# Performance work log

Hardware: AMD Instinct MI355X
Metric: run time of the kernel (lower is better)

The kernel has to match this reference:

```python
import jax, jax.numpy as jnp
import numpy as np

E = 384      # dim_embd
H = 6        # n_heads
D = E // H   # head dim = 64
T_MAX = 256  # block_size
EPS = 1e-5


def setup_inputs() -> dict:
    key = jax.random.key(0)
    ks = jax.random.split(key, 12)
    B, T = 128, 256
    s_in = (1.0 / E) ** 0.5
    s_ff = (1.0 / (4 * E)) ** 0.5
    return {
        "x": jax.random.normal(ks[0], (B, T, E), jnp.float32),
        # per-head projections stacked to match torch concat order: [E, H*D]
        "wq": jax.random.normal(ks[1], (E, E), jnp.float32) * s_in,
        "wk": jax.random.normal(ks[2], (E, E), jnp.float32) * s_in,
        "wv": jax.random.normal(ks[3], (E, E), jnp.float32) * s_in,
        "w_proj": jax.random.normal(ks[4], (E, E), jnp.float32) * s_in,
        "b_proj": jnp.zeros((E,), jnp.float32),
        "w1": jax.random.normal(ks[5], (E, 4 * E), jnp.float32) * s_in,
        "b1": jnp.zeros((4 * E,), jnp.float32),
        "w2": jax.random.normal(ks[6], (4 * E, E), jnp.float32) * s_ff,
        "b2": jnp.zeros((E,), jnp.float32),
        "g1": jnp.ones((E,), jnp.float32),
        "beta1": jnp.zeros((E,), jnp.float32),
        "g2": jnp.ones((E,), jnp.float32),
        "beta2": jnp.zeros((E,), jnp.float32),
    }


def _layernorm(x, g, b):
    mu = jnp.mean(x, axis=-1, keepdims=True)
    var = jnp.mean(jnp.square(x - mu), axis=-1, keepdims=True)
    return (x - mu) * jax.lax.rsqrt(var + EPS) * g + b


def _attention(x, wq, wk, wv, w_proj, b_proj):
    B, T, C = x.shape
    # batched per-head projections: [B,T,H,D]
    q = (x @ wq).reshape(B, T, H, D)
    k = (x @ wk).reshape(B, T, H, D)
    v = (x @ wv).reshape(B, T, H, D)
    # NOTE: original scales by C**-0.5 with C = full embed dim (384)
    scale = C ** (-0.5)
    scores = jnp.einsum("bthd,bshd->bhts", q, k) * scale
    mask = jnp.tril(jnp.ones((T, T), bool))
    scores = jnp.where(mask, scores, -jnp.inf)
    wei = jax.nn.softmax(scores, axis=-1)  # dropout = identity (eval)
    out = jnp.einsum("bhts,bshd->bthd", wei, v).reshape(B, T, C)
    return out @ w_proj + b_proj


def reference(x, wq, wk, wv, w_proj, b_proj, w1, b1, w2, b2, g1, beta1, g2, beta2):
    x = x + _attention(_layernorm(x, g1, beta1), wq, wk, wv, w_proj, b_proj)
    h = _layernorm(x, g2, beta2)
    h = jax.nn.relu(h @ w1 + b1) @ w2 + b2  # dropout = identity (eval)
    return x + h
```

## Files before the change

### kernel.cpp

```cpp
#include <hip/hip_runtime.h>
#include <hip/hip_bf16.h>

typedef __attribute__((ext_vector_type(8))) short bf16x8;
typedef __attribute__((ext_vector_type(4))) float f32x4;

#define MFMA_BF16(a, b, c) __builtin_amdgcn_mfma_f32_16x16x32_bf16((a), (b), (c), 0, 0, 0)

#define E_DIM 384
#define T_SEQ 256
#define B_BATCH 128
#define H_HEADS 6
#define D_HEAD 64
#define NROWS (B_BATCH * T_SEQ)
#define FF_DIM (4 * E_DIM)
#define QKV_LD 1152

__device__ __forceinline__ void load_lds16(const __hip_bfloat16* g, __hip_bfloat16* l) {
    __builtin_amdgcn_global_load_lds(
        (const __attribute__((address_space(1))) void*)g,
        (__attribute__((address_space(3))) void*)l, 16, 0, 0);
}

__device__ __forceinline__ float to_f(float x) { return x; }
__device__ __forceinline__ float to_f(__hip_bfloat16 x) { return __bfloat162float(x); }

__global__ void tcast_all_kernel(const float* __restrict__ wq, const float* __restrict__ wk,
                                 const float* __restrict__ wv, const float* __restrict__ wp,
                                 const float* __restrict__ w1, const float* __restrict__ w2,
                                 __hip_bfloat16* __restrict__ wqkvT, __hip_bfloat16* __restrict__ wpT,
                                 __hip_bfloat16* __restrict__ w1T, __hip_bfloat16* __restrict__ w2T) {
    const int WE = E_DIM * E_DIM;
    const int FE = E_DIM * FF_DIM;
    int idx = blockIdx.x * 256 + threadIdx.x;
    if (idx < 3 * WE) {
        int seg = idx / WE, j = idx - seg * WE;
        const float* W = seg == 0 ? wq : (seg == 1 ? wk : wv);
        int k = j / E_DIM, n = j - k * E_DIM;
        wqkvT[(size_t)seg * WE + (size_t)n * E_DIM + k] = __float2bfloat16(W[j]);
    } else if (idx < 4 * WE) {
        int j = idx - 3 * WE;
        int k = j / E_DIM, n = j - k * E_DIM;
        wpT[(size_t)n * E_DIM + k] = __float2bfloat16(wp[j]);
    } else if (idx < 4 * WE + FE) {
        int j = idx - 4 * WE;
        int k = j / FF_DIM, n = j - k * FF_DIM;
        w1T[(size_t)n * E_DIM + k] = __float2bfloat16(w1[j]);
    } else {
        int j = idx - 4 * WE - FE;
        int k = j / E_DIM, n = j - k * E_DIM;
        w2T[(size_t)n * FF_DIM + k] = __float2bfloat16(w2[j]);
    }
}

template <typename TI>
__global__ __launch_bounds__(256) void ln_kernel(const TI* __restrict__ x,
                                                 const float* __restrict__ g,
                                                 const float* __restrict__ bta,
                                                 __hip_bfloat16* __restrict__ out) {
    int row = blockIdx.x * 4 + (threadIdx.x >> 6);
    int lane = threadIdx.x & 63;
    const TI* xr = x + (size_t)row * E_DIM;
    float vals[6];
    float s = 0.f;
#pragma unroll
    for (int i = 0; i < 3; i++) {
        int c = i * 128 + 2 * lane;
        if constexpr (sizeof(TI) == 4) {
            float2 v = *reinterpret_cast<const float2*>(&xr[c]);
            vals[2 * i] = v.x;
            vals[2 * i + 1] = v.y;
        } else {
            ushort2 u = *reinterpret_cast<const ushort2*>(&xr[c]);
            union { unsigned short us; __hip_bfloat16 h; } a, b2;
            a.us = u.x; b2.us = u.y;
            vals[2 * i] = __bfloat162float(a.h);
            vals[2 * i + 1] = __bfloat162float(b2.h);
        }
        s += vals[2 * i] + vals[2 * i + 1];
    }
#pragma unroll
    for (int off = 1; off < 64; off <<= 1) s += __shfl_xor(s, off, 64);
    float mu = s * (1.f / E_DIM);
    float vv = 0.f;
#pragma unroll
    for (int i = 0; i < 6; i++) {
        float d = vals[i] - mu;
        vv += d * d;
    }
#pragma unroll
    for (int off = 1; off < 64; off <<= 1) vv += __shfl_xor(vv, off, 64);
    float rstd = rsqrtf(vv * (1.f / E_DIM) + 1e-5f);
#pragma unroll
    for (int i = 0; i < 3; i++) {
        int c = i * 128 + 2 * lane;
        float2 gv = *reinterpret_cast<const float2*>(&g[c]);
        float2 bv = *reinterpret_cast<const float2*>(&bta[c]);
        union { ushort2 u; struct { __hip_bfloat16 a, b; } h; } o2;
        o2.h.a = __float2bfloat16((vals[2 * i] - mu) * rstd * gv.x + bv.x);
        o2.h.b = __float2bfloat16((vals[2 * i + 1] - mu) * rstd * gv.y + bv.y);
        *reinterpret_cast<ushort2*>(&out[(size_t)row * E_DIM + c]) = o2.u;
    }
}

template <int EPI, int NW>
__global__ __launch_bounds__(NW * 64, NW == 8 ? 4 : 3) void gemm_kernel(
    const __hip_bfloat16* __restrict__ A, const __hip_bfloat16* __restrict__ BT,
    const float* __restrict__ bias, const void* __restrict__ resid,
    void* __restrict__ outp, int M, int N, int K) {
    constexpr int BM = NW * 32;
    constexpr int T = NW * 64;
    constexpr int BUF = (BM + 128) * 32;
    __shared__ __hip_bfloat16 lds[3 * BUF];
    const int t = threadIdx.x;
    const int w = t >> 6, lane = t & 63;
    const int l16 = lane & 15, lhi = lane >> 4;
    const int wm = w >> 1, wn = w & 1;

    const int nwg = gridDim.x;
    const int bid = blockIdx.x;
    const int cpx = nwg >> 3;
    const int swz = (bid & 7) * cpx + (bid >> 3);
    const int nb = N >> 7;
    const int m0 = (swz / nb) * BM;
    const int n0 = (swz % nb) * 128;

    const int ql = (t & 7) ^ ((t >> 3) & 7);
    const int sr = 2 * (t >> 3) + (ql >> 2);
    const int scol = (ql & 3) * 8;
    const __hip_bfloat16* pa0 = A + (size_t)(m0 + sr) * K + scol;
    const __hip_bfloat16* pa1 = pa0 + (size_t)(T / 4) * K;
    const __hip_bfloat16* pb0 = BT + (size_t)(n0 + sr) * K + scol;
    const __hip_bfloat16* pb1 = pb0 + (size_t)(T / 4) * K;
    const int dstA = t * 8;

    int aoff[4], boff[4];
#pragma unroll
    for (int mr = 0; mr < 4; mr++) {
        int R = wm * 64 + mr * 16 + l16;
        int L = R >> 1;
        int q = (((R & 1) << 2) | lhi) ^ (L & 7);
        aoff[mr] = L * 64 + q * 8;
    }
#pragma unroll
    for (int nr = 0; nr < 4; nr++) {
        int R = wn * 64 + nr * 16 + l16;
        int L = R >> 1;
        int q = (((R & 1) << 2) | lhi) ^ (L & 7);
        boff[nr] = BM * 32 + L * 64 + q * 8;
    }

    f32x4 acc[4][4] = {};
    const int nk = K >> 5;

#define STAGE(sbuf)                                                           \
    {                                                                         \
        __hip_bfloat16* sb_ = &lds[(sbuf) * BUF];                             \
        load_lds16(pa0, sb_ + dstA);                                          \
        load_lds16(pa1, sb_ + T * 8 + dstA);                                  \
        load_lds16(pb0, sb_ + BM * 32 + dstA);                                \
        if constexpr (NW == 4) load_lds16(pb1, sb_ + BM * 32 + T * 8 + dstA); \
        pa0 += 32;                                                            \
        pa1 += 32;                                                            \
        pb0 += 32;                                                            \
        if constexpr (NW == 4) pb1 += 32;                                     \
    }

    STAGE(0);
    STAGE(1);
    int rb = 0, sbx = 2;

    for (int kt = 0; kt < nk; kt++) {
        if (kt + 1 < nk) {
            if constexpr (NW == 8) asm volatile("s_waitcnt vmcnt(3)" ::: "memory");
            else                   asm volatile("s_waitcnt vmcnt(4)" ::: "memory");
        } else {
            asm volatile("s_waitcnt vmcnt(0)" ::: "memory");
        }
        __builtin_amdgcn_s_barrier();
        __builtin_amdgcn_sched_barrier(0);
        if (kt + 2 < nk) STAGE(sbx);
        const __hip_bfloat16* base = &lds[rb * BUF];
        bf16x8 af[4], bg[4];
#pragma unroll
        for (int mr = 0; mr < 4; mr++)
            af[mr] = *reinterpret_cast<const bf16x8*>(base + aoff[mr]);
#pragma unroll
        for (int nr = 0; nr < 4; nr++)
            bg[nr] = *reinterpret_cast<const bf16x8*>(base + boff[nr]);
        __builtin_amdgcn_s_setprio(1);
#pragma unroll
        for (int mr = 0; mr < 4; mr++)
#pragma unroll
            for (int nr = 0; nr < 4; nr++)
                acc[mr][nr] = MFMA_BF16(af[mr], bg[nr], acc[mr][nr]);
        __builtin_amdgcn_s_setprio(0);
        rb = rb == 2 ? 0 : rb + 1;
        sbx = sbx == 2 ? 0 : sbx + 1;
    }
#undef STAGE

    __hip_bfloat16* outb = (__hip_bfloat16*)outp;
    float* outf = (float*)outp;
#pragma unroll
    for (int mr = 0; mr < 4; mr++) {
#pragma unroll
        for (int nr = 0; nr < 4; nr++) {
            const int col = n0 + wn * 64 + nr * 16 + l16;
#pragma unroll
            for (int r = 0; r < 4; r++) {
                const int row = m0 + wm * 64 + mr * 16 + lhi * 4 + r;
                const size_t off = (size_t)row * N + col;
                float v = acc[mr][nr][r];
                if (EPI == 0) {
                    outb[off] = __float2bfloat16(v);
                } else if (EPI == 2) {
                    v += bias[col];
                    outb[off] = __float2bfloat16(v > 0.f ? v : 0.f);
                } else if (EPI == 3) {
                    v += bias[col] + ((const float*)resid)[off];
                    outb[off] = __float2bfloat16(v);
                } else {
                    v += bias[col] + to_f(((const __hip_bfloat16*)resid)[off]);
                    outf[off] = v;
                }
            }
        }
    }
}

__global__ __launch_bounds__(256, 2) void attn_kernel(
    const __hip_bfloat16* __restrict__ qkv, __hip_bfloat16* __restrict__ o) {
    __shared__ __hip_bfloat16 Ks[T_SEQ * 64];
    __shared__ __hip_bfloat16 VTs[64 * 256];
    __shared__ __hip_bfloat16 Ps[4 * 2048];

    const int bh = blockIdx.x;
    const int b = bh / H_HEADS, h = bh - b * H_HEADS;
    const int t = threadIdx.x;
    const int w = t >> 6, lane = t & 63;
    const int l16 = lane & 15, lhi = lane >> 4;
    const int l8 = l16 & 7;
    const size_t rbase = (size_t)b * T_SEQ;
    const int qoff = h * D_HEAD, koff = E_DIM + h * D_HEAD, voff = 2 * E_DIM + h * D_HEAD;
    const float qscale = 0.051031036307982884f * 1.4426950408889634f;

#pragma unroll
    for (int i = 0; i < 8; i++) {
        int idx = i * 256 + t;
        int r = idx >> 3;
        int c8 = idx & 7;
        load_lds16(qkv + (rbase + r) * QKV_LD + koff + ((c8 ^ (r & 7)) << 3),
                   &Ks[idx * 8]);
    }
#pragma unroll
    for (int i = 0; i < 8; i++) {
        int idx = i * 256 + t;
        int r = idx >> 3, d0 = (idx & 7) * 8;
        uint4 val = *reinterpret_cast<const uint4*>(qkv + (rbase + r) * QKV_LD + voff + d0);
        const __hip_bfloat16* p8 = reinterpret_cast<const __hip_bfloat16*>(&val);
        int slot = r >> 3, rin = r & 7;
#pragma unroll
        for (int j = 0; j < 8; j++) {
            int d = d0 + j;
            VTs[d * 256 + ((slot ^ (d & 7)) << 3) + rin] = p8[j];
        }
    }
    __syncthreads();

#pragma unroll
    for (int cp = 0; cp < 2; cp++) {
        const int c = cp ? 7 - w : w;
        bf16x8 qf[2][2];
#pragma unroll
        for (int mr = 0; mr < 2; mr++)
#pragma unroll
            for (int kk = 0; kk < 2; kk++)
                qf[mr][kk] = *reinterpret_cast<const bf16x8*>(
                    qkv + (rbase + c * 32 + mr * 16 + l16) * QKV_LD + qoff + kk * 32 + lhi * 8);

        float mstate[2] = {-1e30f, -1e30f};
        float lstate[2] = {0.f, 0.f};
        f32x4 oacc[2][4] = {};

        const int njt = (c >> 1) + 1;
        for (int jt = 0; jt < njt; jt++) {
            const bool diag = (jt == (c >> 1));
            f32x4 s[2][4] = {};
#pragma unroll
            for (int kk = 0; kk < 2; kk++) {
                bf16x8 kf[4];
#pragma unroll
                for (int nr = 0; nr < 4; nr++) {
                    int R = jt * 64 + nr * 16 + l16;
                    kf[nr] = *reinterpret_cast<const bf16x8*>(
                        &Ks[R * 64 + (((kk << 2) + lhi) ^ l8) * 8]);
                }
#pragma unroll
                for (int mr = 0; mr < 2; mr++)
#pragma unroll
                    for (int nr = 0; nr < 4; nr++)
                        s[mr][nr] = MFMA_BF16(kf[nr], qf[mr][kk], s[mr][nr]);
            }
#pragma unroll
            for (int mr = 0; mr < 2; mr++) {
                const int qrow = c * 32 + mr * 16 + l16;
                float pv[4][4];
                float mx = -1e30f;
#pragma unroll
                for (int nr = 0; nr < 4; nr++)
#pragma unroll
                    for (int r = 0; r < 4; r++) {
                        int kcol = jt * 64 + nr * 16 + lhi * 4 + r;
                        float val = s[mr][nr][r] * qscale;
                        if (diag && kcol > qrow) val = -1e30f;
                        pv[nr][r] = val;
                        mx = fmaxf(mx, val);
                    }
                mx = fmaxf(mx, __shfl_xor(mx, 16, 64));
                mx = fmaxf(mx, __shfl_xor(mx, 32, 64));
                float mold = mstate[mr];
                float mnew = fmaxf(mold, mx);
                float corr = exp2f(mold - mnew);
                float psum = 0.f;
#pragma unroll
                for (int nr = 0; nr < 4; nr++)
#pragma unroll
                    for (int r = 0; r < 4; r++) {
                        float p = exp2f(pv[nr][r] - mnew);
                        pv[nr][r] = p;
                        psum += p;
                    }
                psum += __shfl_xor(psum, 16, 64);
                psum += __shfl_xor(psum, 32, 64);
                lstate[mr] = lstate[mr] * corr + psum;
                mstate[mr] = mnew;
#pragma unroll
                for (int r = 0; r < 4; r++) {
                    float cT = __shfl(corr, lhi * 4 + r, 64);
#pragma unroll
                    for (int dr = 0; dr < 4; dr++) oacc[mr][dr][r] *= cT;
                }
#pragma unroll
                for (int nr = 0; nr < 4; nr++)
#pragma unroll
                    for (int r = 0; r < 4; r++) {
                        int q = mr * 16 + l16;
                        int kc = nr * 16 + lhi * 4 + r;
                        Ps[w * 2048 + q * 64 + (((kc >> 3) ^ (q & 7)) << 3) + (kc & 7)] =
                            __float2bfloat16(pv[nr][r]);
                    }
            }
#pragma unroll
            for (int kk = 0; kk < 2; kk++) {
                bf16x8 pa[2], vbf[4];
#pragma unroll
                for (int mr = 0; mr < 2; mr++) {
                    int row = mr * 16 + l16;
                    pa[mr] = *reinterpret_cast<const bf16x8*>(
                        &Ps[w * 2048 + row * 64 + (((kk << 2) + lhi) ^ l8) * 8]);
                }
#pragma unroll
                for (int dr = 0; dr < 4; dr++) {
                    int d = dr * 16 + l16;
                    int slot = (jt << 3) + (kk << 2) + lhi;
                    vbf[dr] = *reinterpret_cast<const bf16x8*>(
                        &VTs[d * 256 + ((slot ^ l8) << 3)]);
                }
#pragma unroll
                for (int mr = 0; mr < 2; mr++)
#pragma unroll
                    for (int dr = 0; dr < 4; dr++)
                        oacc[mr][dr] = MFMA_BF16(pa[mr], vbf[dr], oacc[mr][dr]);
            }
        }

#pragma unroll
        for (int mr = 0; mr < 2; mr++) {
            float rl = 1.f / lstate[mr];
#pragma unroll
            for (int r = 0; r < 4; r++) {
                float rlT = __shfl(rl, lhi * 4 + r, 64);
                int row = c * 32 + mr * 16 + lhi * 4 + r;
#pragma unroll
                for (int dr = 0; dr < 4; dr++)
                    o[(rbase + row) * E_DIM + h * D_HEAD + dr * 16 + l16] =
                        __float2bfloat16(oacc[mr][dr][r] * rlT);
            }
        }
    }
}

extern "C" void kernel_launch(void* const* d_in, const int* in_sizes, int n_in,
                              void* d_out, int out_size, void* d_ws, size_t ws_size,
                              hipStream_t stream) {
    const float* x      = (const float*)d_in[0];
    const float* wq     = (const float*)d_in[1];
    const float* wk     = (const float*)d_in[2];
    const float* wv     = (const float*)d_in[3];
    const float* w_proj = (const float*)d_in[4];
    const float* b_proj = (const float*)d_in[5];
    const float* w1     = (const float*)d_in[6];
    const float* b1     = (const float*)d_in[7];
    const float* w2     = (const float*)d_in[8];
    const float* b2     = (const float*)d_in[9];
    const float* g1     = (const float*)d_in[10];
    const float* bt1    = (const float*)d_in[11];
    const float* g2     = (const float*)d_in[12];
    const float* bt2    = (const float*)d_in[13];
    float* out = (float*)d_out;

    char* ws = (char*)d_ws;
    size_t off = 0;
    auto alloc = [&](size_t bytes) {
        void* p = ws + off;
        off += (bytes + 255) & ~(size_t)255;
        return p;
    };
    const size_t wElems = E_DIM * E_DIM;
    const size_t fElems = E_DIM * FF_DIM;
    const size_t actElems = (size_t)NROWS * E_DIM;
    __hip_bfloat16* wqkvT = (__hip_bfloat16*)alloc(3 * wElems * 2);
    __hip_bfloat16* wpT   = (__hip_bfloat16*)alloc(wElems * 2);
    __hip_bfloat16* w1T   = (__hip_bfloat16*)alloc(fElems * 2);
    __hip_bfloat16* w2T   = (__hip_bfloat16*)alloc(fElems * 2);
    __hip_bfloat16* lnb   = (__hip_bfloat16*)alloc(actElems * 2);
    __hip_bfloat16* x2b   = (__hip_bfloat16*)alloc(actElems * 2);
    __hip_bfloat16* qkv   = (__hip_bfloat16*)alloc(3 * actElems * 2);
    __hip_bfloat16* ab    = (__hip_bfloat16*)alloc(actElems * 2);
    __hip_bfloat16* h1    = qkv;

    tcast_all_kernel<<<6912, 256, 0, stream>>>(wq, wk, wv, w_proj, w1, w2,
                                               wqkvT, wpT, w1T, w2T);

    ln_kernel<float><<<NROWS / 4, 256, 0, stream>>>(x, g1, bt1, lnb);

    gemm_kernel<0, 8><<<(NROWS / 256) * (QKV_LD / 128), 512, 0, stream>>>(
        lnb, wqkvT, nullptr, nullptr, qkv, NROWS, QKV_LD, E_DIM);

    attn_kernel<<<B_BATCH * H_HEADS, 256, 0, stream>>>(qkv, ab);

    gemm_kernel<3, 4><<<(NROWS / 128) * (E_DIM / 128), 256, 0, stream>>>(
        ab, wpT, b_proj, x, x2b, NROWS, E_DIM, E_DIM);

    ln_kernel<__hip_bfloat16><<<NROWS / 4, 256, 0, stream>>>(x2b, g2, bt2, lnb);

    gemm_kernel<2, 8><<<(NROWS / 256) * (FF_DIM / 128), 512, 0, stream>>>(
        lnb, w1T, b1, nullptr, h1, NROWS, FF_DIM, E_DIM);

    gemm_kernel<4, 4><<<(NROWS / 128) * (E_DIM / 128), 256, 0, stream>>>(
        h1, w2T, b2, x2b, out, NROWS, E_DIM, FF_DIM);
}
```

Baseline: 232.8 us.

## Add ping-pong double-buffered 256x128 GEMM for QKV and FFN1 projections

Introduces a new 8-wave GEMM kernel with a 64-wide K tile, double-buffered LDS, and global-to-LDS prefetch split across two MFMA half-steps with barriers and s_setprio to interleave loads and matrix ops. It replaces the generic gemm_kernel for the QKV projection and the first FFN layer. Occupancy drops to one workgroup per CU because of the larger LDS footprint, in exchange for fewer sync points per K and better overlap of memory with MFMA. The epilogue writes scalar bf16 stores rather than any vectorized path.

Result: slower. 257.6 us (+10.6%).

```diff
diff --git a/kernel.cpp b/kernel.cpp
--- a/kernel.cpp
+++ b/kernel.cpp
@@ -102,6 +102,148 @@
     }
 }
 
+template <int EPI>
+__global__ __launch_bounds__(512, 1) void gemm8p_kernel(
+    const __hip_bfloat16* __restrict__ A, const __hip_bfloat16* __restrict__ BT,
+    const float* __restrict__ bias, void* __restrict__ outp,
+    int M, int N, int K) {
+    __shared__ __hip_bfloat16 lds[2 * 24576];
+    const int t = threadIdx.x;
+    const int w = t >> 6, lane = t & 63;
+    const int l16 = lane & 15, lhi = lane >> 4;
+    const int wm = w >> 1, wn = w & 1;
+
+    const int nwg = gridDim.x;
+    const int bid = blockIdx.x;
+    const int cpx = nwg >> 3;
+    const int swz = (bid & 7) * cpx + (bid >> 3);
+    const int nb = N >> 7;
+    const int m0 = (swz / nb) * 256;
+    const int n0 = (swz % nb) * 128;
+
+    const int sr = t >> 3;
+    const int scol = (((t & 7) ^ (sr & 7)) << 3);
+    const __hip_bfloat16* pa[4];
+    const __hip_bfloat16* pb[2];
+#pragma unroll
+    for (int c = 0; c < 4; c++) pa[c] = A + (size_t)(m0 + c * 64 + sr) * K + scol;
+#pragma unroll
+    for (int c = 0; c < 2; c++) pb[c] = BT + (size_t)(n0 + c * 64 + sr) * K + scol;
+    const int dstu = t * 8;
+
+    int aoff[2][4], boff[2][4];
+#pragma unroll
+    for (int kk = 0; kk < 2; kk++) {
+#pragma unroll
+        for (int mr = 0; mr < 4; mr++) {
+            int R = wm * 64 + mr * 16 + l16;
+            aoff[kk][mr] = R * 64 + (((kk * 4 + lhi) ^ (R & 7)) << 3);
+        }
+#pragma unroll
+        for (int nr = 0; nr < 4; nr++) {
+            int R = wn * 64 + nr * 16 + l16;
+            boff[kk][nr] = 16384 + R * 64 + (((kk * 4 + lhi) ^ (R & 7)) << 3);
+        }
+    }
+
+    f32x4 acc[4][4] = {};
+    const int nt = K >> 6;
+
+#pragma unroll
+    for (int c = 0; c < 4; c++) { load_lds16(pa[c], &lds[c * 4096 + dstu]); pa[c] += 64; }
+#pragma unroll
+    for (int c = 0; c < 2; c++) { load_lds16(pb[c], &lds[16384 + c * 4096 + dstu]); pb[c] += 64; }
+    asm volatile("s_waitcnt vmcnt(0)" ::: "memory");
+    __builtin_amdgcn_s_barrier();
+
+    int cur = 0;
+    for (int kt = 0; kt < nt; kt++) {
+        const bool pf = (kt + 1 < nt);
+        const __hip_bfloat16* base = &lds[cur * 24576];
+        __hip_bfloat16* nbuf = &lds[(cur ^ 1) * 24576];
+
+        {
+            bf16x8 af[4], bg[4];
+#pragma unroll
+            for (int mr = 0; mr < 4; mr++)
+                af[mr] = *reinterpret_cast<const bf16x8*>(base + aoff[0][mr]);
+#pragma unroll
+            for (int nr = 0; nr < 4; nr++)
+                bg[nr] = *reinterpret_cast<const bf16x8*>(base + boff[0][nr]);
+            if (pf) {
+#pragma unroll
+                for (int c = 0; c < 3; c++) {
+                    load_lds16(pa[c], nbuf + c * 4096 + dstu);
+                    pa[c] += 64;
+                }
+            }
+            __builtin_amdgcn_s_barrier();
+            asm volatile("s_waitcnt lgkmcnt(0)" ::: "memory");
+            __builtin_amdgcn_sched_barrier(0);
+            __builtin_amdgcn_s_setprio(1);
+#pragma unroll
+            for (int mr = 0; mr < 4; mr++)
+#pragma unroll
+                for (int nr = 0; nr < 4; nr++)
+                    acc[mr][nr] = MFMA_BF16(af[mr], bg[nr], acc[mr][nr]);
+            __builtin_amdgcn_s_setprio(0);
+            __builtin_amdgcn_s_barrier();
+        }
+        {
+            bf16x8 af[4], bg[4];
+#pragma unroll
+            for (int mr = 0; mr < 4; mr++)
+                af[mr] = *reinterpret_cast<const bf16x8*>(base + aoff[1][mr]);
+#pragma unroll
+            for (int nr = 0; nr < 4; nr++)
+                bg[nr] = *reinterpret_cast<const bf16x8*>(base + boff[1][nr]);
+            if (pf) {
+                load_lds16(pa[3], nbuf + 3 * 4096 + dstu);
+                pa[3] += 64;
+#pragma unroll
+                for (int c = 0; c < 2; c++) {
+                    load_lds16(pb[c], nbuf + 16384 + c * 4096 + dstu);
+                    pb[c] += 64;
+                }
+            }
+            __builtin_amdgcn_s_barrier();
+            asm volatile("s_waitcnt lgkmcnt(0)" ::: "memory");
+            __builtin_amdgcn_sched_barrier(0);
+            __builtin_amdgcn_s_setprio(1);
+#pragma unroll
+            for (int mr = 0; mr < 4; mr++)
+#pragma unroll
+                for (int nr = 0; nr < 4; nr++)
+                    acc[mr][nr] = MFMA_BF16(af[mr], bg[nr], acc[mr][nr]);
+            __builtin_amdgcn_s_setprio(0);
+            if (pf) asm volatile("s_waitcnt vmcnt(0)" ::: "memory");
+            __builtin_amdgcn_s_barrier();
+        }
+        cur ^= 1;
+    }
+
+    __hip_bfloat16* outb = (__hip_bfloat16*)outp;
+#pragma unroll
+    for (int mr = 0; mr < 4; mr++) {
+#pragma unroll
+        for (int nr = 0; nr < 4; nr++) {
+            const int col = n0 + wn * 64 + nr * 16 + l16;
+#pragma unroll
+            for (int r = 0; r < 4; r++) {
+                const int row = m0 + wm * 64 + mr * 16 + lhi * 4 + r;
+                const size_t off = (size_t)row * N + col;
+                float v = acc[mr][nr][r];
+                if (EPI == 0) {
+                    outb[off] = __float2bfloat16(v);
+                } else {
+                    v += bias[col];
+                    outb[off] = __float2bfloat16(v > 0.f ? v : 0.f);
+                }
+            }
+        }
+    }
+}
+
 template <int EPI, int NW>
 __global__ __launch_bounds__(NW * 64, NW == 8 ? 4 : 3) void gemm_kernel(
     const __hip_bfloat16* __restrict__ A, const __hip_bfloat16* __restrict__ BT,
@@ -434,8 +576,8 @@
 
     ln_kernel<float><<<NROWS / 4, 256, 0, stream>>>(x, g1, bt1, lnb);
 
-    gemm_kernel<0, 8><<<(NROWS / 256) * (QKV_LD / 128), 512, 0, stream>>>(
-        lnb, wqkvT, nullptr, nullptr, qkv, NROWS, QKV_LD, E_DIM);
+    gemm8p_kernel<0><<<(NROWS / 256) * (QKV_LD / 128), 512, 0, stream>>>(
+        lnb, wqkvT, nullptr, qkv, NROWS, QKV_LD, E_DIM);
 
     attn_kernel<<<B_BATCH * H_HEADS, 256, 0, stream>>>(qkv, ab);
 
@@ -444,8 +586,8 @@
 
     ln_kernel<__hip_bfloat16><<<NROWS / 4, 256, 0, stream>>>(x2b, g2, bt2, lnb);
 
-    gemm_kernel<2, 8><<<(NROWS / 256) * (FF_DIM / 128), 512, 0, stream>>>(
-        lnb, w1T, b1, nullptr, h1, NROWS, FF_DIM, E_DIM);
+    gemm8p_kernel<2><<<(NROWS / 256) * (FF_DIM / 128), 512, 0, stream>>>(
+        lnb, w1T, b1, h1, NROWS, FF_DIM, E_DIM);
 
     gemm_kernel<4, 4><<<(NROWS / 128) * (E_DIM / 128), 256, 0, stream>>>(
         h1, w2T, b2, x2b, out, NROWS, E_DIM, FF_DIM);
```
